# Kernel optimization log

Measured on AMD Instinct MI355X. Metric: run time of the kernel, lower is better.

## Reference

```python
import jax, jax.numpy as jnp
import numpy as np

SMOOTH = 9.0
EPS = 1e-8
LEAK = 0.1  # LeakyReLU slope used by SCAN_attention


def setup_inputs() -> dict:
    key = jax.random.key(0)
    k1, k2, k3, k4 = jax.random.split(key, 4)
    n_img, n_reg, d = 256, 36, 1024
    n_cap, max_w = 256, 60
    imgs = jax.random.normal(k1, (n_img, n_reg, d), dtype=jnp.float32)
    caps = jax.random.normal(k2, (n_cap, max_w, d), dtype=jnp.float32)
    img_lens = jax.random.randint(k3, (n_img,), 1, n_reg + 1, dtype=jnp.int32)
    cap_lens = jax.random.randint(k4, (n_cap,), 5, max_w + 1, dtype=jnp.int32)
    return {"imgs": imgs, "caps": caps, "img_lens": img_lens, "cap_lens": cap_lens}


def reference(imgs, caps, img_lens, cap_lens):
    # imgs: (I, R, D); caps: (C, W, D); cap_lens: (C,)
    C, W, D = caps.shape
    mask = (jnp.arange(W)[None, :] < cap_lens[:, None]).astype(caps.dtype)  # (C, W)
    # Zero padded words: equivalent to the per-caption slicing in the torch loop
    q = caps * mask[:, :, None]

    # SCAN attention, vectorized over captions and images.
    # raw scores: context . query^T  -> (C, I, W, R)
    s = jnp.einsum('cwd,ird->ciwr', q, imgs)
    s = jnp.where(s >= 0, s, LEAK * s)  # LeakyReLU(0.1)
    # l2norm over the word dim (padded words contribute exactly 0)
    norm = jnp.sqrt(jnp.sum(s * s, axis=2, keepdims=True)) + EPS
    s = s / norm
    attn = jax.nn.softmax(s * SMOOTH, axis=3)  # softmax over regions
    wctx = jnp.einsum('ciwr,ird->ciwd', attn, imgs)  # (C, I, W, D)

    # cosine similarity over feature dim
    w12 = jnp.einsum('cwd,ciwd->ciw', q, wctx)
    w1 = jnp.sqrt(jnp.sum(q * q, axis=-1))[:, None, :]          # (C, 1, W)
    w2 = jnp.sqrt(jnp.sum(wctx * wctx, axis=-1))                # (C, I, W)
    sim = w12 / jnp.maximum(w1 * w2, EPS)                       # (C, I, W)

    # masked mean over valid words (matches per-caption mean over n_word)
    col = jnp.sum(sim * mask[:, None, :], axis=2) / cap_lens.astype(sim.dtype)[:, None]
    return col.T  # (n_image, n_caption)
```

## Files before the change

kernel.cpp:

```cpp
#include <hip/hip_runtime.h>


#define NIMG 256
#define NREG 36
#define DIM 1024
#define NCAP 256
#define MAXW 60
#define WPAD 64

typedef short bf16x8 __attribute__((ext_vector_type(8)));
typedef float f32x4 __attribute__((ext_vector_type(4)));

__device__ __forceinline__ unsigned short f2bf(float f) {
  unsigned u = __float_as_uint(f);
  u += 0x7FFF + ((u >> 16) & 1);
  return (unsigned short)(u >> 16);
}

__global__ void k_prep_w1(const float* __restrict__ caps, const int* __restrict__ cap_lens,
                          float* __restrict__ w1) {
  const int bid = blockIdx.x;
  const int c = bid >> 6;
  const int w = bid & 63;
  const int t = threadIdx.x;
  const bool valid = (w < MAXW) && (w < cap_lens[c]);
  float4 v = make_float4(0.f, 0.f, 0.f, 0.f);
  if (valid) v = *reinterpret_cast<const float4*>(caps + ((size_t)c * MAXW + w) * DIM + t * 4);
  float ss = v.x * v.x + v.y * v.y + v.z * v.z + v.w * v.w;
#pragma unroll
  for (int m = 1; m <= 32; m <<= 1) ss += __shfl_xor(ss, m);
  __shared__ float part[4];
  if ((t & 63) == 0) part[t >> 6] = ss;
  __syncthreads();
  if (t == 0) w1[bid] = sqrtf(part[0] + part[1] + part[2] + part[3]);
}

__global__ void k_prep_caps_frag(const float* __restrict__ caps, const int* __restrict__ cap_lens,
                                 unsigned short* __restrict__ qbfF) {
  const int k32 = blockIdx.x;
  const int c = blockIdx.y;
  const int t = threadIdx.x;
  const int mt = t >> 6;
  const int lane = t & 63;
  const int m = mt * 16 + (lane & 15);
  const int k0 = k32 * 32 + (lane >> 4) * 8;
  const int clen = cap_lens[c];
  float4 v0 = make_float4(0.f, 0.f, 0.f, 0.f), v1 = v0;
  if (m < clen && m < MAXW) {
    const float* src = caps + ((size_t)c * MAXW + m) * DIM + k0;
    v0 = *reinterpret_cast<const float4*>(src);
    v1 = *reinterpret_cast<const float4*>(src + 4);
  }
  ushort4 o0, o1;
  o0.x = f2bf(v0.x); o0.y = f2bf(v0.y); o0.z = f2bf(v0.z); o0.w = f2bf(v0.w);
  o1.x = f2bf(v1.x); o1.y = f2bf(v1.y); o1.z = f2bf(v1.z); o1.w = f2bf(v1.w);
  unsigned short* dst = qbfF + ((size_t)(((c * 32 + k32) * 4 + mt) * 64 + lane)) * 8;
  *reinterpret_cast<ushort4*>(dst) = o0;
  *reinterpret_cast<ushort4*>(dst + 4) = o1;
}

__global__ void k_prep_imgs_frag(const float* __restrict__ imgs,
                                 unsigned short* __restrict__ ibfF) {
  const int k32 = blockIdx.x;
  const int i = blockIdx.y;
  const int t = threadIdx.x;
  const int nt = t >> 6;
  const int lane = t & 63;
  const int r = nt * 16 + (lane & 15);
  const int k0 = k32 * 32 + (lane >> 4) * 8;
  float4 v0 = make_float4(0.f, 0.f, 0.f, 0.f), v1 = v0;
  if (r < NREG) {
    const float* src = imgs + ((size_t)i * NREG + r) * DIM + k0;
    v0 = *reinterpret_cast<const float4*>(src);
    v1 = *reinterpret_cast<const float4*>(src + 4);
  }
  ushort4 o0, o1;
  o0.x = f2bf(v0.x); o0.y = f2bf(v0.y); o0.z = f2bf(v0.z); o0.w = f2bf(v0.w);
  o1.x = f2bf(v1.x); o1.y = f2bf(v1.y); o1.z = f2bf(v1.z); o1.w = f2bf(v1.w);
  unsigned short* dst = ibfF + ((size_t)(((i * 32 + k32) * 3 + nt) * 64 + lane)) * 8;
  *reinterpret_cast<ushort4*>(dst) = o0;
  *reinterpret_cast<ushort4*>(dst + 4) = o1;
}

__global__ void k_gram_mfma(const float* __restrict__ imgs,
                            const unsigned short* __restrict__ ibfF,
                            unsigned short* __restrict__ gbf,
                            float* __restrict__ gdiag) {
  const int i = blockIdx.x;
  const int lane = threadIdx.x & 63;
  const int l15 = lane & 15;
  const int quad = lane >> 4;

  float* dg = gdiag + (size_t)i * 48;
#pragma unroll
  for (int r0 = 0; r0 < 36; r0 += 4) {
    const int r = r0 + quad;
    const float* row = imgs + ((size_t)i * NREG + r) * DIM;
    float ss = 0.f;
#pragma unroll
    for (int p = 0; p < 16; ++p) {
      float4 v = *reinterpret_cast<const float4*>(row + p * 64 + l15 * 4);
      ss += v.x * v.x + v.y * v.y + v.z * v.z + v.w * v.w;
    }
    ss += __shfl_xor(ss, 1); ss += __shfl_xor(ss, 2);
    ss += __shfl_xor(ss, 4); ss += __shfl_xor(ss, 8);
    if (l15 == 0) dg[r] = ss;
  }
  if (lane < 12) dg[36 + lane] = 0.f;

  const unsigned short* base = ibfF + ((size_t)i * 32 * 3) * 512 + lane * 8;
  const f32x4 zero4 = {0.f, 0.f, 0.f, 0.f};
  f32x4 acc[3][3];
#pragma unroll
  for (int na = 0; na < 3; ++na)
#pragma unroll
    for (int nb = 0; nb < 3; ++nb) acc[na][nb] = zero4;
  bf16x8 f[2][3];
#pragma unroll
  for (int nt = 0; nt < 3; ++nt)
    f[0][nt] = *reinterpret_cast<const bf16x8*>(base + (size_t)nt * 512);
#pragma unroll
  for (int k32 = 0; k32 < 32; ++k32) {
    if (k32 + 1 < 32) {
      const int nb_ = (k32 + 1) & 1;
#pragma unroll
      for (int nt = 0; nt < 3; ++nt)
        f[nb_][nt] = *reinterpret_cast<const bf16x8*>(base + ((size_t)(k32 + 1) * 3 + nt) * 512);
    }
    const int b = k32 & 1;
#pragma unroll
    for (int na = 0; na < 3; ++na)
#pragma unroll
      for (int nb = 0; nb < 3; ++nb)
        acc[na][nb] = __builtin_amdgcn_mfma_f32_16x16x32_bf16(f[b][na], f[b][nb], acc[na][nb], 0, 0, 0);
  }
  unsigned short* g = gbf + (size_t)i * (48 * 64);
#pragma unroll
  for (int na = 0; na < 3; ++na)
#pragma unroll
    for (int nb = 0; nb < 3; ++nb)
#pragma unroll
      for (int rg = 0; rg < 4; ++rg) {
        const int r = na * 16 + quad * 4 + rg;
        const int c = nb * 16 + l15;
        g[r * 64 + c] = (r == c) ? (unsigned short)0 : f2bf(acc[na][nb][rg]);
      }
  for (int idx = lane; idx < 96; idx += 64) {
    const int r = idx >> 1, half = idx & 1;
    *reinterpret_cast<uint4*>(g + r * 64 + 48 + half * 8) = make_uint4(0, 0, 0, 0);
  }
}

template <int MLIM>
__device__ __forceinline__ void kloopT(const unsigned short* __restrict__ aBase,
                                       const unsigned short* __restrict__ bBase,
                                       f32x4 (&acc)[3][4]) {
  bf16x8 fa[3][MLIM], fb[3][3];
  auto load = [&](int k32, int buf) __attribute__((always_inline)) {
#pragma unroll
    for (int nt = 0; nt < 3; ++nt)
      fb[buf][nt] = *reinterpret_cast<const bf16x8*>(bBase + ((size_t)k32 * 3 + nt) * 512);
#pragma unroll
    for (int mt = 0; mt < MLIM; ++mt)
      fa[buf][mt] = *reinterpret_cast<const bf16x8*>(aBase + ((size_t)k32 * 4 + mt) * 512);
  };
  auto compute = [&](int buf) __attribute__((always_inline)) {
#pragma unroll
    for (int mt = 0; mt < MLIM; ++mt)
#pragma unroll
      for (int nt = 0; nt < 3; ++nt)
        acc[nt][mt] = __builtin_amdgcn_mfma_f32_16x16x32_bf16(fb[buf][nt], fa[buf][mt], acc[nt][mt], 0, 0, 0);
  };
  load(0, 0);
  load(1, 1);
#pragma unroll
  for (int k32 = 0; k32 < 32; ++k32) {
    if (k32 + 2 < 32) load(k32 + 2, (k32 + 2) % 3);
    __builtin_amdgcn_sched_barrier(0);
    compute(k32 % 3);
  }
}

__launch_bounds__(256, 3)
__global__ void k_main(const unsigned short* __restrict__ qbfF,
                       const unsigned short* __restrict__ ibfF,
                       const float* __restrict__ w1,
                       const unsigned short* __restrict__ gbf,
                       const float* __restrict__ gdiag,
                       const int* __restrict__ cap_lens,
                       float* __restrict__ out) {
  __shared__ struct {
    unsigned short attn[4][64 * 64];
    float w12[4][64];
    float w2d[4][64];
    float w2x[4][64];
  } lds;
  const int tid = threadIdx.x;
  const int lane = tid & 63;
  const int wv = tid >> 6;
  const int l15 = lane & 15;
  const int quad = lane >> 4;
  const int flat = blockIdx.y * (NIMG / 2) + blockIdx.x;
  const int xcd = flat & 7;
  const int idx = flat >> 3;
  const int bx = xcd * 16 + (idx & 15);
  const int by = idx >> 4;
  const int i0 = bx * 2;
  const int c = by * 2 + (wv & 1);
  const int img = i0 + (wv >> 1);
  const int clen = cap_lens[c];
  const int mlim = (clen + 15) >> 4;

  f32x4 acc[3][4];
  const f32x4 zero4 = {0.f, 0.f, 0.f, 0.f};
#pragma unroll
  for (int nt = 0; nt < 3; ++nt)
#pragma unroll
    for (int mt = 0; mt < 4; ++mt) acc[nt][mt] = zero4;

  const unsigned short* aBase = qbfF + ((size_t)c * 32 * 4) * 512 + lane * 8;
  const unsigned short* bBase = ibfF + ((size_t)img * 32 * 3) * 512 + lane * 8;

  switch (mlim) {
    case 1: kloopT<1>(aBase, bBase, acc); break;
    case 2: kloopT<2>(aBase, bBase, acc); break;
    case 3: kloopT<3>(aBase, bBase, acc); break;
    default: kloopT<4>(aBase, bBase, acc); break;
  }

  {
    uint4* ab = reinterpret_cast<uint4*>(&lds.attn[wv][0]);
    const uint4 z4 = make_uint4(0, 0, 0, 0);
    for (int j = lane; j < 512; j += 64) ab[j] = z4;
  }

  const float* dg = gdiag + (size_t)img * 48;
  float dv[3][4];
#pragma unroll
  for (int nt = 0; nt < 3; ++nt)
#pragma unroll
    for (int rg = 0; rg < 4; ++rg)
      dv[nt][rg] = dg[nt * 16 + quad * 4 + rg];

  float scale[3][4];
#pragma unroll
  for (int nt = 0; nt < 3; ++nt)
#pragma unroll
    for (int rg = 0; rg < 4; ++rg) {
      float p = 0.f;
#pragma unroll
      for (int mt = 0; mt < 4; ++mt)
        if (mt < mlim) {
          const float s = acc[nt][mt][rg];
          const float l = s < 0.f ? 0.1f * s : s;
          p += l * l;
        }
      p += __shfl_xor(p, 1); p += __shfl_xor(p, 2);
      p += __shfl_xor(p, 4); p += __shfl_xor(p, 8);
      scale[nt][rg] = 9.0f / (sqrtf(p) + 1e-8f);
    }

  float a_all[4][3][4];
  float inv4[4];
#pragma unroll
  for (int mt = 0; mt < 4; ++mt) {
    if (mt >= mlim) continue;
    float sm = 0.f, wp = 0.f, dd = 0.f;
#pragma unroll
    for (int nt = 0; nt < 3; ++nt) {
      const bool rvalid = (nt < 2) || (quad == 0);
#pragma unroll
      for (int rg = 0; rg < 4; ++rg) {
        const float s = acc[nt][mt][rg];
        const float l = s < 0.f ? 0.1f * s : s;
        const float ee = rvalid ? __expf(l * scale[nt][rg]) : 0.f;
        a_all[mt][nt][rg] = ee;
        sm += ee;
        wp += ee * s;
        dd += ee * ee * dv[nt][rg];
      }
    }
    sm += __shfl_xor(sm, 16); sm += __shfl_xor(sm, 32);
    wp += __shfl_xor(wp, 16); wp += __shfl_xor(wp, 32);
    dd += __shfl_xor(dd, 16); dd += __shfl_xor(dd, 32);
    const float inv = 1.0f / sm;
    inv4[mt] = inv;
    const int w = mt * 16 + l15;
    const int key = l15 & 7;
    unsigned short* arow = &lds.attn[wv][w * 64];
#pragma unroll
    for (int nt = 0; nt < 3; ++nt)
#pragma unroll
      for (int rg = 0; rg < 4; ++rg) {
        const int r = nt * 16 + quad * 4 + rg;
        arow[(((r >> 3) ^ key) << 3) + (r & 7)] = f2bf(a_all[mt][nt][rg] * inv);
      }
    if (quad == 0) { lds.w12[wv][w] = wp * inv; lds.w2d[wv][w] = dd * inv * inv; }
  }

  bf16x8 gfrag[3][2];
#pragma unroll
  for (int nt = 0; nt < 3; ++nt)
#pragma unroll
    for (int ks = 0; ks < 2; ++ks)
      gfrag[nt][ks] = *reinterpret_cast<const bf16x8*>(
          gbf + ((size_t)img * 48 + nt * 16 + l15) * 64 + ((ks * 4 + quad) << 3));
#pragma unroll
  for (int mt = 0; mt < 4; ++mt) {
    if (mt >= mlim) continue;
    bf16x8 af[2];
#pragma unroll
    for (int ks = 0; ks < 2; ++ks)
      af[ks] = *reinterpret_cast<const bf16x8*>(
          &lds.attn[wv][(mt * 16 + l15) * 64 + (((ks * 4 + quad) ^ (l15 & 7)) << 3)]);
    f32x4 Yt[3] = {zero4, zero4, zero4};
#pragma unroll
    for (int nt = 0; nt < 3; ++nt)
#pragma unroll
      for (int ks = 0; ks < 2; ++ks)
        Yt[nt] = __builtin_amdgcn_mfma_f32_16x16x32_bf16(gfrag[nt][ks], af[ks], Yt[nt], 0, 0, 0);
    float p = 0.f;
#pragma unroll
    for (int nt = 0; nt < 3; ++nt)
#pragma unroll
      for (int rg = 0; rg < 4; ++rg)
        p += a_all[mt][nt][rg] * Yt[nt][rg];
    p *= inv4[mt];
    p += __shfl_xor(p, 16); p += __shfl_xor(p, 32);
    if (quad == 0) lds.w2x[wv][mt * 16 + l15] = p;
  }

  float simv = 0.f;
  if (lane < clen) {
    const float w2sq = fmaxf(lds.w2x[wv][lane] + lds.w2d[wv][lane], 0.f);
    const float w2v = sqrtf(w2sq);
    const float w12v = lds.w12[wv][lane];
    const float w1v = w1[(size_t)c * WPAD + lane];
    simv = w12v / fmaxf(w1v * w2v, 1e-8f);
  }
  simv += __shfl_xor(simv, 1);
  simv += __shfl_xor(simv, 2);
  simv += __shfl_xor(simv, 4);
  simv += __shfl_xor(simv, 8);
  simv += __shfl_xor(simv, 16);
  simv += __shfl_xor(simv, 32);
  if (lane == 0) out[(size_t)img * NCAP + c] = simv / (float)clen;
}

extern "C" void kernel_launch(void* const* d_in, const int* in_sizes, int n_in,
                              void* d_out, int out_size, void* d_ws, size_t ws_size,
                              hipStream_t stream) {
  const float* imgs = (const float*)d_in[0];
  const float* caps = (const float*)d_in[1];
  const int* cap_lens = (const int*)d_in[3];
  float* out = (float*)d_out;

  char* ws = (char*)d_ws;
  const size_t QBF_B = (size_t)NCAP * 32 * 4 * 512 * 2;
  const size_t IBF_B = (size_t)NIMG * 32 * 3 * 512 * 2;
  const size_t W1_B = (size_t)NCAP * WPAD * 4;
  const size_t GBF_B = (size_t)NIMG * 48 * 64 * 2;
  unsigned short* qbfF = (unsigned short*)ws;
  unsigned short* ibfF = (unsigned short*)(ws + QBF_B);
  float* w1 = (float*)(ws + QBF_B + IBF_B);
  unsigned short* gbf = (unsigned short*)(ws + QBF_B + IBF_B + W1_B);
  float* gdiag = (float*)(ws + QBF_B + IBF_B + W1_B + GBF_B);

  k_prep_w1<<<NCAP * WPAD, 256, 0, stream>>>(caps, cap_lens, w1);
  k_prep_caps_frag<<<dim3(32, NCAP), 256, 0, stream>>>(caps, cap_lens, qbfF);
  k_prep_imgs_frag<<<dim3(32, NIMG), 192, 0, stream>>>(imgs, ibfF);
  k_gram_mfma<<<NIMG, 64, 0, stream>>>(imgs, ibfF, gbf, gdiag);
  k_main<<<dim3(NIMG / 2, NCAP / 2), 256, 0, stream>>>(qbfF, ibfF, w1, gbf, gdiag, cap_lens, out);
}
```

Before: 522.6 us.

## Stage main-loop operands in shared LDS via async global loads and sort captions by length

In the main kernel, operand fragments are now loaded cooperatively into double-buffered LDS with global_load_lds. Each wave stages one caption's or one image's fragments, and the other waves in the block reuse them instead of each wave fetching its own copy from global memory. A new sort kernel builds a permutation of captions by length, so the two captions sharing a block have similar lengths and similar trip counts. The LDS staging buffer is unioned with the attention buffer and the occupancy hint is raised to 4. The cost is a __syncthreads per k-step plus an extra small launch, and the deep register prefetch pipeline is gone.

```diff
diff --git a/kernel.cpp b/kernel.cpp
--- a/kernel.cpp
+++ b/kernel.cpp
@@ -15,6 +15,11 @@
   unsigned u = __float_as_uint(f);
   u += 0x7FFF + ((u >> 16) & 1);
   return (unsigned short)(u >> 16);
+}
+
+__device__ __forceinline__ void gll16(const unsigned short* g, unsigned short* l) {
+  __builtin_amdgcn_global_load_lds((const __attribute__((address_space(1))) void*)g,
+                                   (__attribute__((address_space(3))) void*)l, 16, 0, 0);
 }
 
 __global__ void k_prep_w1(const float* __restrict__ caps, const int* __restrict__ cap_lens,
@@ -33,6 +38,17 @@
   if ((t & 63) == 0) part[t >> 6] = ss;
   __syncthreads();
   if (t == 0) w1[bid] = sqrtf(part[0] + part[1] + part[2] + part[3]);
+}
+
+__global__ void k_sort(const int* __restrict__ cap_lens, int* __restrict__ perm) {
+  const int i = threadIdx.x;
+  const int li = cap_lens[i];
+  int r = 0;
+  for (int j = 0; j < NCAP; ++j) {
+    const int lj = cap_lens[j];
+    r += (lj < li) || (lj == li && j < i);
+  }
+  perm[r] = i;
 }
 
 __global__ void k_prep_caps_frag(const float* __restrict__ caps, const int* __restrict__ cap_lens,
@@ -151,50 +167,56 @@
   }
 }
 
+#define BUFO 7168
 template <int MLIM>
-__device__ __forceinline__ void kloopT(const unsigned short* __restrict__ aBase,
-                                       const unsigned short* __restrict__ bBase,
+__device__ __forceinline__ void kloopS(const unsigned short* __restrict__ sSrc,
+                                       unsigned short* __restrict__ sDst,
+                                       const int sCnt, const size_t sK32,
+                                       const unsigned short* __restrict__ aLds,
+                                       const unsigned short* __restrict__ bLds,
                                        f32x4 (&acc)[3][4]) {
-  bf16x8 fa[3][MLIM], fb[3][3];
-  auto load = [&](int k32, int buf) __attribute__((always_inline)) {
+  for (int j = 0; j < sCnt; ++j)
+    gll16(sSrc + j * 512, sDst + j * 512);
+  __syncthreads();
+#pragma unroll 2
+  for (int t = 0; t < 32; ++t) {
+    const int cur = t & 1;
+    if (t + 1 < 32) {
+      unsigned short* d = sDst + (cur ^ 1) * BUFO;
+      const unsigned short* s = sSrc + (size_t)(t + 1) * sK32;
+      for (int j = 0; j < sCnt; ++j)
+        gll16(s + j * 512, d + j * 512);
+    }
+    bf16x8 fb[3], fa[MLIM];
 #pragma unroll
     for (int nt = 0; nt < 3; ++nt)
-      fb[buf][nt] = *reinterpret_cast<const bf16x8*>(bBase + ((size_t)k32 * 3 + nt) * 512);
+      fb[nt] = *reinterpret_cast<const bf16x8*>(bLds + cur * BUFO + nt * 512);
 #pragma unroll
     for (int mt = 0; mt < MLIM; ++mt)
-      fa[buf][mt] = *reinterpret_cast<const bf16x8*>(aBase + ((size_t)k32 * 4 + mt) * 512);
-  };
-  auto compute = [&](int buf) __attribute__((always_inline)) {
+      fa[mt] = *reinterpret_cast<const bf16x8*>(aLds + cur * BUFO + mt * 512);
 #pragma unroll
     for (int mt = 0; mt < MLIM; ++mt)
 #pragma unroll
       for (int nt = 0; nt < 3; ++nt)
-        acc[nt][mt] = __builtin_amdgcn_mfma_f32_16x16x32_bf16(fb[buf][nt], fa[buf][mt], acc[nt][mt], 0, 0, 0);
-  };
-  load(0, 0);
-  load(1, 1);
-#pragma unroll
-  for (int k32 = 0; k32 < 32; ++k32) {
-    if (k32 + 2 < 32) load(k32 + 2, (k32 + 2) % 3);
-    __builtin_amdgcn_sched_barrier(0);
-    compute(k32 % 3);
-  }
-}
-
-__launch_bounds__(256, 3)
+        acc[nt][mt] = __builtin_amdgcn_mfma_f32_16x16x32_bf16(fb[nt], fa[mt], acc[nt][mt], 0, 0, 0);
+    __syncthreads();
+  }
+}
+
+__launch_bounds__(256, 4)
 __global__ void k_main(const unsigned short* __restrict__ qbfF,
                        const unsigned short* __restrict__ ibfF,
                        const float* __restrict__ w1,
                        const unsigned short* __restrict__ gbf,
                        const float* __restrict__ gdiag,
                        const int* __restrict__ cap_lens,
+                       const int* __restrict__ perm,
                        float* __restrict__ out) {
-  __shared__ struct {
-    unsigned short attn[4][64 * 64];
-    float w12[4][64];
-    float w2d[4][64];
-    float w2x[4][64];
-  } lds;
+  __shared__ union {
+    unsigned short stg[2][BUFO];
+    unsigned short attn[4][4096];
+  } u;
+  __shared__ float w12s[4][64], w2ds[4][64], w2xs[4][64];
   const int tid = threadIdx.x;
   const int lane = tid & 63;
   const int wv = tid >> 6;
@@ -206,11 +228,33 @@
   const int bx = xcd * 16 + (idx & 15);
   const int by = idx >> 4;
   const int i0 = bx * 2;
-  const int c = by * 2 + (wv & 1);
+  const int cA = perm[2 * by], cB = perm[2 * by + 1];
+  const int c = (wv & 1) ? cB : cA;
   const int img = i0 + (wv >> 1);
   const int clen = cap_lens[c];
   const int mlim = (clen + 15) >> 4;
 
+  const unsigned short* sSrc;
+  unsigned short* sDst;
+  int sCnt;
+  size_t sK32;
+  if (wv == 0) {
+    sSrc = qbfF + (size_t)cA * 32 * 4 * 512; sDst = &u.stg[0][0];
+    sCnt = (cap_lens[cA] + 15) >> 4; sK32 = 4 * 512;
+  } else if (wv == 1) {
+    sSrc = qbfF + (size_t)cB * 32 * 4 * 512; sDst = &u.stg[0][2048];
+    sCnt = (cap_lens[cB] + 15) >> 4; sK32 = 4 * 512;
+  } else if (wv == 2) {
+    sSrc = ibfF + (size_t)i0 * 32 * 3 * 512; sDst = &u.stg[0][4096];
+    sCnt = 3; sK32 = 3 * 512;
+  } else {
+    sSrc = ibfF + (size_t)(i0 + 1) * 32 * 3 * 512; sDst = &u.stg[0][5632];
+    sCnt = 3; sK32 = 3 * 512;
+  }
+  sSrc += lane * 8;
+  const unsigned short* aLds = &u.stg[0][(wv & 1) * 2048] + lane * 8;
+  const unsigned short* bLds = &u.stg[0][4096 + (wv >> 1) * 1536] + lane * 8;
+
   f32x4 acc[3][4];
   const f32x4 zero4 = {0.f, 0.f, 0.f, 0.f};
 #pragma unroll
@@ -218,18 +262,15 @@
 #pragma unroll
     for (int mt = 0; mt < 4; ++mt) acc[nt][mt] = zero4;
 
-  const unsigned short* aBase = qbfF + ((size_t)c * 32 * 4) * 512 + lane * 8;
-  const unsigned short* bBase = ibfF + ((size_t)img * 32 * 3) * 512 + lane * 8;
-
   switch (mlim) {
-    case 1: kloopT<1>(aBase, bBase, acc); break;
-    case 2: kloopT<2>(aBase, bBase, acc); break;
-    case 3: kloopT<3>(aBase, bBase, acc); break;
-    default: kloopT<4>(aBase, bBase, acc); break;
+    case 1: kloopS<1>(sSrc, sDst, sCnt, sK32, aLds, bLds, acc); break;
+    case 2: kloopS<2>(sSrc, sDst, sCnt, sK32, aLds, bLds, acc); break;
+    case 3: kloopS<3>(sSrc, sDst, sCnt, sK32, aLds, bLds, acc); break;
+    default: kloopS<4>(sSrc, sDst, sCnt, sK32, aLds, bLds, acc); break;
   }
 
   {
-    uint4* ab = reinterpret_cast<uint4*>(&lds.attn[wv][0]);
+    uint4* ab = reinterpret_cast<uint4*>(&u.attn[wv][0]);
     const uint4 z4 = make_uint4(0, 0, 0, 0);
     for (int j = lane; j < 512; j += 64) ab[j] = z4;
   }
@@ -287,7 +328,7 @@
     inv4[mt] = inv;
     const int w = mt * 16 + l15;
     const int key = l15 & 7;
-    unsigned short* arow = &lds.attn[wv][w * 64];
+    unsigned short* arow = &u.attn[wv][w * 64];
 #pragma unroll
     for (int nt = 0; nt < 3; ++nt)
 #pragma unroll
@@ -295,7 +336,7 @@
         const int r = nt * 16 + quad * 4 + rg;
         arow[(((r >> 3) ^ key) << 3) + (r & 7)] = f2bf(a_all[mt][nt][rg] * inv);
       }
-    if (quad == 0) { lds.w12[wv][w] = wp * inv; lds.w2d[wv][w] = dd * inv * inv; }
+    if (quad == 0) { w12s[wv][w] = wp * inv; w2ds[wv][w] = dd * inv * inv; }
   }
 
   bf16x8 gfrag[3][2];
@@ -312,7 +353,7 @@
 #pragma unroll
     for (int ks = 0; ks < 2; ++ks)
       af[ks] = *reinterpret_cast<const bf16x8*>(
-          &lds.attn[wv][(mt * 16 + l15) * 64 + (((ks * 4 + quad) ^ (l15 & 7)) << 3)]);
+          &u.attn[wv][(mt * 16 + l15) * 64 + (((ks * 4 + quad) ^ (l15 & 7)) << 3)]);
     f32x4 Yt[3] = {zero4, zero4, zero4};
 #pragma unroll
     for (int nt = 0; nt < 3; ++nt)
@@ -327,14 +368,14 @@
         p += a_all[mt][nt][rg] * Yt[nt][rg];
     p *= inv4[mt];
     p += __shfl_xor(p, 16); p += __shfl_xor(p, 32);
-    if (quad == 0) lds.w2x[wv][mt * 16 + l15] = p;
+    if (quad == 0) w2xs[wv][mt * 16 + l15] = p;
   }
 
   float simv = 0.f;
   if (lane < clen) {
-    const float w2sq = fmaxf(lds.w2x[wv][lane] + lds.w2d[wv][lane], 0.f);
+    const float w2sq = fmaxf(w2xs[wv][lane] + w2ds[wv][lane], 0.f);
     const float w2v = sqrtf(w2sq);
-    const float w12v = lds.w12[wv][lane];
+    const float w12v = w12s[wv][lane];
     const float w1v = w1[(size_t)c * WPAD + lane];
     simv = w12v / fmaxf(w1v * w2v, 1e-8f);
   }
@@ -360,15 +401,18 @@
   const size_t IBF_B = (size_t)NIMG * 32 * 3 * 512 * 2;
   const size_t W1_B = (size_t)NCAP * WPAD * 4;
   const size_t GBF_B = (size_t)NIMG * 48 * 64 * 2;
+  const size_t GD_B = (size_t)NIMG * 48 * 4;
   unsigned short* qbfF = (unsigned short*)ws;
   unsigned short* ibfF = (unsigned short*)(ws + QBF_B);
   float* w1 = (float*)(ws + QBF_B + IBF_B);
   unsigned short* gbf = (unsigned short*)(ws + QBF_B + IBF_B + W1_B);
   float* gdiag = (float*)(ws + QBF_B + IBF_B + W1_B + GBF_B);
+  int* perm = (int*)(ws + QBF_B + IBF_B + W1_B + GBF_B + GD_B);
 
   k_prep_w1<<<NCAP * WPAD, 256, 0, stream>>>(caps, cap_lens, w1);
+  k_sort<<<1, NCAP, 0, stream>>>(cap_lens, perm);
   k_prep_caps_frag<<<dim3(32, NCAP), 256, 0, stream>>>(caps, cap_lens, qbfF);
   k_prep_imgs_frag<<<dim3(32, NIMG), 192, 0, stream>>>(imgs, ibfF);
   k_gram_mfma<<<NIMG, 64, 0, stream>>>(imgs, ibfF, gbf, gdiag);
-  k_main<<<dim3(NIMG / 2, NCAP / 2), 256, 0, stream>>>(qbfF, ibfF, w1, gbf, gdiag, cap_lens, out);
-}
+  k_main<<<dim3(NIMG / 2, NCAP / 2), 256, 0, stream>>>(qbfF, ibfF, w1, gbf, gdiag, cap_lens, perm, out);
+}
```

Result: slower. 639.9 us (+22.4%).

## Sort captions by length, fuse word-norm prep, pack attention as bf16 pairs

Applied to the files above, without the earlier changes.

Adds a single-block rank sort of captions by length so each k_main block pairs captions of similar length. This is meant to cut the divergence and wasted MFMA tiles that come from the per-wave mlim switch when the two captions in a block differ. The separate w1 norm kernel is dropped: squared norms are accumulated with atomics inside the caption fragment prep, and the square root is taken in k_main. Attention weights are kept in registers as packed bf16 pairs instead of fp32, which lowers register pressure and uses 32-bit LDS stores, at the cost of slightly lower precision in the w2 cross term.

```diff
diff --git a/kernel.cpp b/kernel.cpp
--- a/kernel.cpp
+++ b/kernel.cpp
@@ -17,26 +17,23 @@
   return (unsigned short)(u >> 16);
 }
 
-__global__ void k_prep_w1(const float* __restrict__ caps, const int* __restrict__ cap_lens,
-                          float* __restrict__ w1) {
-  const int bid = blockIdx.x;
-  const int c = bid >> 6;
-  const int w = bid & 63;
-  const int t = threadIdx.x;
-  const bool valid = (w < MAXW) && (w < cap_lens[c]);
-  float4 v = make_float4(0.f, 0.f, 0.f, 0.f);
-  if (valid) v = *reinterpret_cast<const float4*>(caps + ((size_t)c * MAXW + w) * DIM + t * 4);
-  float ss = v.x * v.x + v.y * v.y + v.z * v.z + v.w * v.w;
-#pragma unroll
-  for (int m = 1; m <= 32; m <<= 1) ss += __shfl_xor(ss, m);
-  __shared__ float part[4];
-  if ((t & 63) == 0) part[t >> 6] = ss;
-  __syncthreads();
-  if (t == 0) w1[bid] = sqrtf(part[0] + part[1] + part[2] + part[3]);
+__global__ void k_sort(const int* __restrict__ cap_lens, int* __restrict__ perm,
+                       float* __restrict__ w1sq) {
+  const int i = threadIdx.x;
+#pragma unroll
+  for (int j = 0; j < WPAD; ++j) w1sq[i * WPAD + j] = 0.f;
+  const int li = cap_lens[i];
+  int r = 0;
+  for (int j = 0; j < NCAP; ++j) {
+    const int lj = cap_lens[j];
+    r += (lj < li) || (lj == li && j < i);
+  }
+  perm[r] = i;
 }
 
 __global__ void k_prep_caps_frag(const float* __restrict__ caps, const int* __restrict__ cap_lens,
-                                 unsigned short* __restrict__ qbfF) {
+                                 unsigned short* __restrict__ qbfF,
+                                 float* __restrict__ w1sq) {
   const int k32 = blockIdx.x;
   const int c = blockIdx.y;
   const int t = threadIdx.x;
@@ -51,6 +48,11 @@
     v0 = *reinterpret_cast<const float4*>(src);
     v1 = *reinterpret_cast<const float4*>(src + 4);
   }
+  float ss = v0.x * v0.x + v0.y * v0.y + v0.z * v0.z + v0.w * v0.w
+           + v1.x * v1.x + v1.y * v1.y + v1.z * v1.z + v1.w * v1.w;
+  ss += __shfl_xor(ss, 16);
+  ss += __shfl_xor(ss, 32);
+  if ((lane >> 4) == 0 && ss != 0.f) atomicAdd(&w1sq[(size_t)c * WPAD + m], ss);
   ushort4 o0, o1;
   o0.x = f2bf(v0.x); o0.y = f2bf(v0.y); o0.z = f2bf(v0.z); o0.w = f2bf(v0.w);
   o1.x = f2bf(v1.x); o1.y = f2bf(v1.y); o1.z = f2bf(v1.z); o1.w = f2bf(v1.w);
@@ -184,13 +186,14 @@
 __launch_bounds__(256, 3)
 __global__ void k_main(const unsigned short* __restrict__ qbfF,
                        const unsigned short* __restrict__ ibfF,
-                       const float* __restrict__ w1,
+                       const float* __restrict__ w1sq,
                        const unsigned short* __restrict__ gbf,
                        const float* __restrict__ gdiag,
                        const int* __restrict__ cap_lens,
+                       const int* __restrict__ perm,
                        float* __restrict__ out) {
   __shared__ struct {
-    unsigned short attn[4][64 * 64];
+    unsigned short attn[4][4096];
     float w12[4][64];
     float w2d[4][64];
     float w2x[4][64];
@@ -206,7 +209,8 @@
   const int bx = xcd * 16 + (idx & 15);
   const int by = idx >> 4;
   const int i0 = bx * 2;
-  const int c = by * 2 + (wv & 1);
+  const int cA = perm[2 * by], cB = perm[2 * by + 1];
+  const int c = (wv & 1) ? cB : cA;
   const int img = i0 + (wv >> 1);
   const int clen = cap_lens[c];
   const int mlim = (clen + 15) >> 4;
@@ -260,11 +264,11 @@
       scale[nt][rg] = 9.0f / (sqrtf(p) + 1e-8f);
     }
 
-  float a_all[4][3][4];
-  float inv4[4];
+  unsigned a_pk[4][3][2];
 #pragma unroll
   for (int mt = 0; mt < 4; ++mt) {
     if (mt >= mlim) continue;
+    float ee[3][4];
     float sm = 0.f, wp = 0.f, dd = 0.f;
 #pragma unroll
     for (int nt = 0; nt < 3; ++nt) {
@@ -273,27 +277,30 @@
       for (int rg = 0; rg < 4; ++rg) {
         const float s = acc[nt][mt][rg];
         const float l = s < 0.f ? 0.1f * s : s;
-        const float ee = rvalid ? __expf(l * scale[nt][rg]) : 0.f;
-        a_all[mt][nt][rg] = ee;
-        sm += ee;
-        wp += ee * s;
-        dd += ee * ee * dv[nt][rg];
+        const float e0 = rvalid ? __expf(l * scale[nt][rg]) : 0.f;
+        ee[nt][rg] = e0;
+        sm += e0;
+        wp += e0 * s;
+        dd += e0 * e0 * dv[nt][rg];
       }
     }
     sm += __shfl_xor(sm, 16); sm += __shfl_xor(sm, 32);
     wp += __shfl_xor(wp, 16); wp += __shfl_xor(wp, 32);
     dd += __shfl_xor(dd, 16); dd += __shfl_xor(dd, 32);
     const float inv = 1.0f / sm;
-    inv4[mt] = inv;
     const int w = mt * 16 + l15;
     const int key = l15 & 7;
     unsigned short* arow = &lds.attn[wv][w * 64];
 #pragma unroll
     for (int nt = 0; nt < 3; ++nt)
 #pragma unroll
-      for (int rg = 0; rg < 4; ++rg) {
-        const int r = nt * 16 + quad * 4 + rg;
-        arow[(((r >> 3) ^ key) << 3) + (r & 7)] = f2bf(a_all[mt][nt][rg] * inv);
+      for (int pr = 0; pr < 2; ++pr) {
+        const unsigned b0 = f2bf(ee[nt][2 * pr] * inv);
+        const unsigned b1 = f2bf(ee[nt][2 * pr + 1] * inv);
+        const unsigned pk = b0 | (b1 << 16);
+        a_pk[mt][nt][pr] = pk;
+        const int r0 = nt * 16 + quad * 4 + 2 * pr;
+        *reinterpret_cast<unsigned*>(&arow[(((r0 >> 3) ^ key) << 3) + (r0 & 7)]) = pk;
       }
     if (quad == 0) { lds.w12[wv][w] = wp * inv; lds.w2d[wv][w] = dd * inv * inv; }
   }
@@ -323,9 +330,12 @@
 #pragma unroll
     for (int nt = 0; nt < 3; ++nt)
 #pragma unroll
-      for (int rg = 0; rg < 4; ++rg)
-        p += a_all[mt][nt][rg] * Yt[nt][rg];
-    p *= inv4[mt];
+      for (int pr = 0; pr < 2; ++pr) {
+        const unsigned pk = a_pk[mt][nt][pr];
+        const float a0 = __uint_as_float(pk << 16);
+        const float a1 = __uint_as_float(pk & 0xffff0000u);
+        p += a0 * Yt[nt][2 * pr] + a1 * Yt[nt][2 * pr + 1];
+      }
     p += __shfl_xor(p, 16); p += __shfl_xor(p, 32);
     if (quad == 0) lds.w2x[wv][mt * 16 + l15] = p;
   }
@@ -335,7 +345,7 @@
     const float w2sq = fmaxf(lds.w2x[wv][lane] + lds.w2d[wv][lane], 0.f);
     const float w2v = sqrtf(w2sq);
     const float w12v = lds.w12[wv][lane];
-    const float w1v = w1[(size_t)c * WPAD + lane];
+    const float w1v = sqrtf(w1sq[(size_t)c * WPAD + lane]);
     simv = w12v / fmaxf(w1v * w2v, 1e-8f);
   }
   simv += __shfl_xor(simv, 1);
@@ -360,15 +370,17 @@
   const size_t IBF_B = (size_t)NIMG * 32 * 3 * 512 * 2;
   const size_t W1_B = (size_t)NCAP * WPAD * 4;
   const size_t GBF_B = (size_t)NIMG * 48 * 64 * 2;
+  const size_t GD_B = (size_t)NIMG * 48 * 4;
   unsigned short* qbfF = (unsigned short*)ws;
   unsigned short* ibfF = (unsigned short*)(ws + QBF_B);
-  float* w1 = (float*)(ws + QBF_B + IBF_B);
+  float* w1sq = (float*)(ws + QBF_B + IBF_B);
   unsigned short* gbf = (unsigned short*)(ws + QBF_B + IBF_B + W1_B);
   float* gdiag = (float*)(ws + QBF_B + IBF_B + W1_B + GBF_B);
-
-  k_prep_w1<<<NCAP * WPAD, 256, 0, stream>>>(caps, cap_lens, w1);
-  k_prep_caps_frag<<<dim3(32, NCAP), 256, 0, stream>>>(caps, cap_lens, qbfF);
+  int* perm = (int*)(ws + QBF_B + IBF_B + W1_B + GBF_B + GD_B);
+
+  k_sort<<<1, NCAP, 0, stream>>>(cap_lens, perm, w1sq);
+  k_prep_caps_frag<<<dim3(32, NCAP), 256, 0, stream>>>(caps, cap_lens, qbfF, w1sq);
   k_prep_imgs_frag<<<dim3(32, NIMG), 192, 0, stream>>>(imgs, ibfF);
   k_gram_mfma<<<NIMG, 64, 0, stream>>>(imgs, ibfF, gbf, gdiag);
-  k_main<<<dim3(NIMG / 2, NCAP / 2), 256, 0, stream>>>(qbfF, ibfF, w1, gbf, gdiag, cap_lens, out);
-}
+  k_main<<<dim3(NIMG / 2, NCAP / 2), 256, 0, stream>>>(qbfF, ibfF, w1sq, gbf, gdiag, cap_lens, perm, out);
+}
```

Result: slower. 533.2 us (+2.0%).
